# Kernel optimization log

Hardware: AMD Instinct MI355X
Metric: run time of the kernel (lower is better)

The kernel has to match this reference:

```python
import jax, jax.numpy as jnp
import numpy as np

B = 4096       # batch size
DIM = 1024     # feature dim
E = 9          # 8 session experts + 1 default layer (index 8)


def setup_inputs() -> dict:
    key = jax.random.key(0)
    k_x, k_w, k_b, k_i = jax.random.split(key, 4)
    x = jax.random.normal(k_x, (B, DIM), dtype=jnp.float32)
    # Stacked nn.Linear params: W[e] has torch layout [out, in], b[e] is [out].
    # (Original init is identity+zero bias; random values exercise the same math.)
    W = jax.random.normal(k_w, (E, DIM, DIM), dtype=jnp.float32) * (DIM ** -0.5)
    b = jax.random.normal(k_b, (E, DIM), dtype=jnp.float32)
    session_idx = jax.random.randint(k_i, (B,), 0, E, dtype=jnp.int64)
    return {"x": x, "W": W, "b": b, "session_idx": session_idx}


def reference(x, W, b, session_idx):
    # Per-sample keyed linear: out[i] = x[i] @ W[session_idx[i]].T + b[session_idx[i]].
    # Dense formulation: run every expert on every sample (E small), then select.
    # y: [B, E, DIM]
    y = jnp.einsum('bd,eod->beo', x, W) + b[None, :, :]
    out = y[jnp.arange(x.shape[0]), session_idx]  # [B, DIM]
    return out
```

## Files before the change

kernel.cpp:

```cpp
#include <hip/hip_runtime.h>
#include <hip/hip_bf16.h>

#define NE 9
#define NDIM 1024
#define BM 64
#define BN 64
#define BK 64
#define NT (NDIM / BK)
#define NSLOT_MAX 72
#define WPX 144

typedef __attribute__((ext_vector_type(8))) short bf16x8;
typedef __attribute__((ext_vector_type(4))) float f32x4;

__device__ __forceinline__ unsigned pack2_bf16(float a, float b) {
    __hip_bfloat162 h = __float22bfloat162_rn(float2{a, b});
    return *reinterpret_cast<unsigned*>(&h);
}

__device__ __forceinline__ void gload_lds16(const void* g, void* l) {
    __builtin_amdgcn_global_load_lds(
        (const __attribute__((address_space(1))) unsigned int*)g,
        (__attribute__((address_space(3))) unsigned int*)l, 16, 0, 0);
}

__global__ __launch_bounds__(256)
void prep_kernel(const float* __restrict__ W, const int* __restrict__ sidx,
                 unsigned short* __restrict__ Wb,
                 int* __restrict__ perm, int4* __restrict__ desc, int nB) {
    if (blockIdx.x == 0) {
        __shared__ int cnt[NE];
        __shared__ int cur[NE];
        int t = threadIdx.x;
        if (t < NE) cnt[t] = 0;
        __syncthreads();
        for (int i = t; i < nB; i += 256) atomicAdd(&cnt[sidx[i]], 1);
        __syncthreads();
        if (t == 0) {
            int run = 0, s = 0;
            for (int e = 0; e < NE; ++e) {
                cur[e] = run;
                int c = cnt[e];
                for (int m0 = 0; m0 < c; m0 += BM) {
                    desc[s] = make_int4(e, run + m0, min(BM, c - m0), 0);
                    ++s;
                }
                run += c;
            }
            for (; s < NSLOT_MAX; ++s) desc[s] = make_int4(-1, 0, 1, 0);
        }
        __syncthreads();
        for (int i = t; i < nB; i += 256) {
            int p = atomicAdd(&cur[sidx[i]], 1);
            perm[p] = i;
        }
    } else {
        const int NW8 = NE * NDIM * (NDIM / 8);
        const int stride = (gridDim.x - 1) * 256;
        for (int u = (blockIdx.x - 1) * 256 + threadIdx.x; u < NW8; u += stride) {
            const float4* src = (const float4*)W + 2 * (size_t)u;
            float4 a = src[0], c = src[1];
            uint4 o;
            o.x = pack2_bf16(a.x, a.y);
            o.y = pack2_bf16(a.z, a.w);
            o.z = pack2_bf16(c.x, c.y);
            o.w = pack2_bf16(c.z, c.w);
            ((uint4*)Wb)[u] = o;
        }
    }
}

__global__ __launch_bounds__(256, 4)
void gemm_kernel(const float* __restrict__ x,
                 const unsigned short* __restrict__ Wb,
                 const float* __restrict__ bias,
                 const int* __restrict__ perm,
                 const int4* __restrict__ desc,
                 float* __restrict__ out) {
    const int b    = blockIdx.x;
    const int w    = (b & 7) * WPX + (b >> 3);
    const int slot = w >> 4;
    const int n    = w & 15;
    const int4 d   = desc[slot];
    if (d.x < 0) return;
    const int e = d.x, rowstart = d.y, rcnt = d.z;
    const int n0 = n * BN;

    __shared__ __align__(16) unsigned short lds[16384];

    const int t    = threadIdx.x;
    const int wave = t >> 6;
    const int lane = t & 63;
    const int fr   = lane & 15;
    const int fq   = lane >> 4;
    const int wr   = (wave >> 1) * 32;
    const int wc   = (wave & 1) * 32;
    const int xr   = fr & 7;

    const int srow = t >> 3;
    const int c8   = t & 7;
    const int sc   = c8 ^ (srow & 7);

    int lm0 = srow;      if (lm0 >= rcnt) lm0 = rcnt - 1;
    int lm1 = srow + 32; if (lm1 >= rcnt) lm1 = rcnt - 1;
    const float* ap0 = x + (size_t)perm[rowstart + lm0] * NDIM + c8 * 8;
    const float* ap1 = x + (size_t)perm[rowstart + lm1] * NDIM + c8 * 8;
    const unsigned short* bp =
        Wb + ((size_t)e * NDIM + n0 + srow) * NDIM + sc * 8;

    float4 av[4];

#define LOADA(K0)                                                              \
    do {                                                                       \
        av[0] = *(const float4*)(ap0 + (K0));                                  \
        av[1] = *(const float4*)(ap0 + (K0) + 4);                              \
        av[2] = *(const float4*)(ap1 + (K0));                                  \
        av[3] = *(const float4*)(ap1 + (K0) + 4);                              \
    } while (0)

#define CVTA(BUF)                                                              \
    do {                                                                       \
        uint4 o0, o1;                                                          \
        o0.x = pack2_bf16(av[0].x, av[0].y);                                   \
        o0.y = pack2_bf16(av[0].z, av[0].w);                                   \
        o0.z = pack2_bf16(av[1].x, av[1].y);                                   \
        o0.w = pack2_bf16(av[1].z, av[1].w);                                   \
        o1.x = pack2_bf16(av[2].x, av[2].y);                                   \
        o1.y = pack2_bf16(av[2].z, av[2].w);                                   \
        o1.z = pack2_bf16(av[3].x, av[3].y);                                   \
        o1.w = pack2_bf16(av[3].z, av[3].w);                                   \
        *reinterpret_cast<uint4*>(&lds[(BUF) * 4096 + srow * 64 + sc * 8]) = o0;      \
        *reinterpret_cast<uint4*>(&lds[(BUF) * 4096 + (srow + 32) * 64 + sc * 8]) = o1;\
    } while (0)

#define STAGEB(BUF, K0)                                                        \
    do {                                                                       \
        gload_lds16(bp + (K0), &lds[8192 + (BUF) * 4096 + wave * 512]);        \
        gload_lds16(bp + (size_t)32 * NDIM + (K0),                             \
                    &lds[8192 + (BUF) * 4096 + 2048 + wave * 512]);            \
    } while (0)

    f32x4 acc[2][2];
#pragma unroll
    for (int i = 0; i < 2; ++i)
#pragma unroll
        for (int k = 0; k < 2; ++k) acc[i][k] = (f32x4)(0.0f);

    LOADA(0);
    STAGEB(0, 0);
    CVTA(0);
    LOADA(BK);
    __syncthreads();

    for (int tt = 0; tt < NT; ++tt) {
        const int cur = tt & 1;
        if (tt + 1 < NT) STAGEB(cur ^ 1, (tt + 1) * BK);

        const int abase = cur * 4096;
        const int bbase = 8192 + cur * 4096;
#pragma unroll
        for (int kk = 0; kk < 2; ++kk) {
            const int cs = ((kk * 4 + fq) ^ xr) * 8;
            bf16x8 af[2], bfv[2];
#pragma unroll
            for (int mf = 0; mf < 2; ++mf)
                af[mf] = *reinterpret_cast<const bf16x8*>(
                    &lds[abase + (wr + mf * 16 + fr) * 64 + cs]);
#pragma unroll
            for (int nf = 0; nf < 2; ++nf)
                bfv[nf] = *reinterpret_cast<const bf16x8*>(
                    &lds[bbase + (wc + nf * 16 + fr) * 64 + cs]);
#pragma unroll
            for (int mf = 0; mf < 2; ++mf)
#pragma unroll
                for (int nf = 0; nf < 2; ++nf)
                    acc[mf][nf] = __builtin_amdgcn_mfma_f32_16x16x32_bf16(
                        af[mf], bfv[nf], acc[mf][nf], 0, 0, 0);
        }

        if (tt + 1 < NT) {
            CVTA(cur ^ 1);
            if (tt + 2 < NT) LOADA((tt + 2) * BK);
            __syncthreads();
        }
    }
#undef LOADA
#undef CVTA
#undef STAGEB

    float bl[2];
#pragma unroll
    for (int nf = 0; nf < 2; ++nf)
        bl[nf] = bias[e * NDIM + n0 + wc + nf * 16 + fr];

#pragma unroll
    for (int mf = 0; mf < 2; ++mf) {
#pragma unroll
        for (int jr = 0; jr < 4; ++jr) {
            int lm = wr + mf * 16 + fq * 4 + jr;
            if (lm < rcnt) {
                int grow = perm[rowstart + lm];
                float* orow = out + (size_t)grow * NDIM;
#pragma unroll
                for (int nf = 0; nf < 2; ++nf)
                    orow[n0 + wc + nf * 16 + fr] = acc[mf][nf][jr] + bl[nf];
            }
        }
    }
}

__global__ void naive_kernel(const float* __restrict__ x, const float* __restrict__ W,
                             const float* __restrict__ bias,
                             const int* __restrict__ sidx, float* __restrict__ out,
                             int nB) {
    int i = blockIdx.x;
    int c = threadIdx.x + (blockIdx.y << 8);
    if (i >= nB || c >= NDIM) return;
    int e = sidx[i];
    const float* wrow = W + ((size_t)e * NDIM + c) * NDIM;
    const float* xr = x + (size_t)i * NDIM;
    float s = bias[e * NDIM + c];
    for (int k = 0; k < NDIM; ++k) s += xr[k] * wrow[k];
    out[(size_t)i * NDIM + c] = s;
}

extern "C" void kernel_launch(void* const* d_in, const int* in_sizes, int n_in,
                              void* d_out, int out_size, void* d_ws, size_t ws_size,
                              hipStream_t stream) {
    const float* x    = (const float*)d_in[0];
    const float* W    = (const float*)d_in[1];
    const float* bias = (const float*)d_in[2];
    const int*   sidx = (const int*)d_in[3];
    float*       out  = (float*)d_out;

    const int nB = in_sizes[3];

    char* wsb = (char*)d_ws;
    size_t p_desc = (size_t)nB * 4;
    size_t p_wb   = ((p_desc + NSLOT_MAX * 16 + 511) / 512) * 512;
    size_t need   = p_wb + (size_t)NE * NDIM * NDIM * 2;

    if (ws_size < need) {
        dim3 g(nB, NDIM / 256);
        naive_kernel<<<g, 256, 0, stream>>>(x, W, bias, sidx, out, nB);
        return;
    }

    int*  perm = (int*)wsb;
    int4* desc = (int4*)(wsb + p_desc);
    unsigned short* Wb = (unsigned short*)(wsb + p_wb);

    prep_kernel<<<1024, 256, 0, stream>>>(W, sidx, Wb, perm, desc, nB);

    gemm_kernel<<<NSLOT_MAX * 16, 256, 0, stream>>>(x, Wb, bias, perm, desc, out);
}
```

Baseline: 52.45 us.

## Replace LDS-staged GEMM with register-direct MFMA loads and pre-converted bf16 x

The prep kernel now also converts x to bf16 in a workspace buffer. The GEMM drops LDS staging and barriers entirely: each wave loads its MFMA operand fragments straight from global memory into registers with a two-stage software prefetch. Tiles grow to 128 rows by 64 columns, and each wave now owns 32 rows by 64 columns. This removes the LDS round trip and the syncthreads, and it halves the slot count. In exchange, operands are no longer shared across waves, so global and L2 traffic per block rises, and every load is an uncoalesced strided 16-byte fragment.

```diff
diff --git a/kernel.cpp b/kernel.cpp
--- a/kernel.cpp
+++ b/kernel.cpp
@@ -3,12 +3,9 @@
 
 #define NE 9
 #define NDIM 1024
-#define BM 64
-#define BN 64
-#define BK 64
-#define NT (NDIM / BK)
-#define NSLOT_MAX 72
-#define WPX 144
+#define SLOT_ROWS 128
+#define NSLOT_MAX 48
+#define SPX (NSLOT_MAX / 8)
 
 typedef __attribute__((ext_vector_type(8))) short bf16x8;
 typedef __attribute__((ext_vector_type(4))) float f32x4;
@@ -18,15 +15,10 @@
     return *reinterpret_cast<unsigned*>(&h);
 }
 
-__device__ __forceinline__ void gload_lds16(const void* g, void* l) {
-    __builtin_amdgcn_global_load_lds(
-        (const __attribute__((address_space(1))) unsigned int*)g,
-        (__attribute__((address_space(3))) unsigned int*)l, 16, 0, 0);
-}
-
 __global__ __launch_bounds__(256)
-void prep_kernel(const float* __restrict__ W, const int* __restrict__ sidx,
-                 unsigned short* __restrict__ Wb,
+void prep_kernel(const float* __restrict__ x, const float* __restrict__ W,
+                 const int* __restrict__ sidx,
+                 unsigned short* __restrict__ xb, unsigned short* __restrict__ Wb,
                  int* __restrict__ perm, int4* __restrict__ desc, int nB) {
     if (blockIdx.x == 0) {
         __shared__ int cnt[NE];
@@ -41,8 +33,8 @@
             for (int e = 0; e < NE; ++e) {
                 cur[e] = run;
                 int c = cnt[e];
-                for (int m0 = 0; m0 < c; m0 += BM) {
-                    desc[s] = make_int4(e, run + m0, min(BM, c - m0), 0);
+                for (int m0 = 0; m0 < c; m0 += SLOT_ROWS) {
+                    desc[s] = make_int4(e, run + m0, min(SLOT_ROWS, c - m0), 0);
                     ++s;
                 }
                 run += c;
@@ -56,154 +48,135 @@
         }
     } else {
         const int NW8 = NE * NDIM * (NDIM / 8);
+        const int NX8 = nB * (NDIM / 8);
+        const int tot = NW8 + NX8;
         const int stride = (gridDim.x - 1) * 256;
-        for (int u = (blockIdx.x - 1) * 256 + threadIdx.x; u < NW8; u += stride) {
-            const float4* src = (const float4*)W + 2 * (size_t)u;
+        for (int u = (blockIdx.x - 1) * 256 + threadIdx.x; u < tot; u += stride) {
+            const float4* src;
+            uint4* dst;
+            if (u < NW8) {
+                src = (const float4*)W + 2 * (size_t)u;
+                dst = (uint4*)Wb + u;
+            } else {
+                size_t v = (size_t)(u - NW8);
+                src = (const float4*)x + 2 * v;
+                dst = (uint4*)xb + v;
+            }
             float4 a = src[0], c = src[1];
             uint4 o;
             o.x = pack2_bf16(a.x, a.y);
             o.y = pack2_bf16(a.z, a.w);
             o.z = pack2_bf16(c.x, c.y);
             o.w = pack2_bf16(c.z, c.w);
-            ((uint4*)Wb)[u] = o;
+            *dst = o;
         }
     }
 }
 
 __global__ __launch_bounds__(256, 4)
-void gemm_kernel(const float* __restrict__ x,
-                 const unsigned short* __restrict__ Wb,
-                 const float* __restrict__ bias,
-                 const int* __restrict__ perm,
-                 const int4* __restrict__ desc,
-                 float* __restrict__ out) {
+void gemm_reg_kernel(const unsigned short* __restrict__ xb,
+                     const unsigned short* __restrict__ Wb,
+                     const float* __restrict__ bias,
+                     const int* __restrict__ perm,
+                     const int4* __restrict__ desc,
+                     float* __restrict__ out) {
     const int b    = blockIdx.x;
-    const int w    = (b & 7) * WPX + (b >> 3);
-    const int slot = w >> 4;
-    const int n    = w & 15;
+    const int xcd  = b & 7;
+    const int loc  = b >> 3;
+    const int slot = xcd * SPX + (loc >> 4);
+    const int n    = loc & 15;
     const int4 d   = desc[slot];
     if (d.x < 0) return;
     const int e = d.x, rowstart = d.y, rcnt = d.z;
-    const int n0 = n * BN;
-
-    __shared__ __align__(16) unsigned short lds[16384];
+    const int n0 = n * 64;
 
     const int t    = threadIdx.x;
     const int wave = t >> 6;
     const int lane = t & 63;
     const int fr   = lane & 15;
     const int fq   = lane >> 4;
-    const int wr   = (wave >> 1) * 32;
-    const int wc   = (wave & 1) * 32;
-    const int xr   = fr & 7;
-
-    const int srow = t >> 3;
-    const int c8   = t & 7;
-    const int sc   = c8 ^ (srow & 7);
-
-    int lm0 = srow;      if (lm0 >= rcnt) lm0 = rcnt - 1;
-    int lm1 = srow + 32; if (lm1 >= rcnt) lm1 = rcnt - 1;
-    const float* ap0 = x + (size_t)perm[rowstart + lm0] * NDIM + c8 * 8;
-    const float* ap1 = x + (size_t)perm[rowstart + lm1] * NDIM + c8 * 8;
-    const unsigned short* bp =
-        Wb + ((size_t)e * NDIM + n0 + srow) * NDIM + sc * 8;
-
-    float4 av[4];
-
-#define LOADA(K0)                                                              \
+    const int ws   = wave * 32;
+
+    const unsigned short* ap0;
+    const unsigned short* ap1;
+    {
+        int lm0 = ws + fr;      if (lm0 >= rcnt) lm0 = rcnt - 1;
+        int lm1 = ws + 16 + fr; if (lm1 >= rcnt) lm1 = rcnt - 1;
+        ap0 = xb + (size_t)perm[rowstart + lm0] * NDIM + fq * 8;
+        ap1 = xb + (size_t)perm[rowstart + lm1] * NDIM + fq * 8;
+    }
+    const unsigned short* bp0 = Wb + ((size_t)e * NDIM + n0 +      fr) * NDIM + fq * 8;
+    const unsigned short* bp1 = bp0 + (size_t)16 * NDIM;
+    const unsigned short* bp2 = bp0 + (size_t)32 * NDIM;
+    const unsigned short* bp3 = bp0 + (size_t)48 * NDIM;
+
+    f32x4 acc[2][4];
+#pragma unroll
+    for (int i = 0; i < 2; ++i)
+#pragma unroll
+        for (int k = 0; k < 4; ++k) acc[i][k] = (f32x4)(0.0f);
+
+    bf16x8 a0_0, a0_1, b0_0, b0_1, b0_2, b0_3;
+    bf16x8 a1_0, a1_1, b1_0, b1_1, b1_2, b1_3;
+
+#define LD0(KK)                                                    \
+    do {                                                           \
+        a0_0 = *(const bf16x8*)(ap0 + (KK));                       \
+        a0_1 = *(const bf16x8*)(ap1 + (KK));                       \
+        b0_0 = *(const bf16x8*)(bp0 + (KK));                       \
+        b0_1 = *(const bf16x8*)(bp1 + (KK));                       \
+        b0_2 = *(const bf16x8*)(bp2 + (KK));                       \
+        b0_3 = *(const bf16x8*)(bp3 + (KK));                       \
+    } while (0)
+#define LD1(KK)                                                    \
+    do {                                                           \
+        a1_0 = *(const bf16x8*)(ap0 + (KK));                       \
+        a1_1 = *(const bf16x8*)(ap1 + (KK));                       \
+        b1_0 = *(const bf16x8*)(bp0 + (KK));                       \
+        b1_1 = *(const bf16x8*)(bp1 + (KK));                       \
+        b1_2 = *(const bf16x8*)(bp2 + (KK));                       \
+        b1_3 = *(const bf16x8*)(bp3 + (KK));                       \
+    } while (0)
+#define MM(A0, A1, B0, B1, B2, B3)                                             \
     do {                                                                       \
-        av[0] = *(const float4*)(ap0 + (K0));                                  \
-        av[1] = *(const float4*)(ap0 + (K0) + 4);                              \
-        av[2] = *(const float4*)(ap1 + (K0));                                  \
-        av[3] = *(const float4*)(ap1 + (K0) + 4);                              \
+        acc[0][0] = __builtin_amdgcn_mfma_f32_16x16x32_bf16(A0, B0, acc[0][0], 0, 0, 0); \
+        acc[0][1] = __builtin_amdgcn_mfma_f32_16x16x32_bf16(A0, B1, acc[0][1], 0, 0, 0); \
+        acc[0][2] = __builtin_amdgcn_mfma_f32_16x16x32_bf16(A0, B2, acc[0][2], 0, 0, 0); \
+        acc[0][3] = __builtin_amdgcn_mfma_f32_16x16x32_bf16(A0, B3, acc[0][3], 0, 0, 0); \
+        acc[1][0] = __builtin_amdgcn_mfma_f32_16x16x32_bf16(A1, B0, acc[1][0], 0, 0, 0); \
+        acc[1][1] = __builtin_amdgcn_mfma_f32_16x16x32_bf16(A1, B1, acc[1][1], 0, 0, 0); \
+        acc[1][2] = __builtin_amdgcn_mfma_f32_16x16x32_bf16(A1, B2, acc[1][2], 0, 0, 0); \
+        acc[1][3] = __builtin_amdgcn_mfma_f32_16x16x32_bf16(A1, B3, acc[1][3], 0, 0, 0); \
     } while (0)
 
-#define CVTA(BUF)                                                              \
-    do {                                                                       \
-        uint4 o0, o1;                                                          \
-        o0.x = pack2_bf16(av[0].x, av[0].y);                                   \
-        o0.y = pack2_bf16(av[0].z, av[0].w);                                   \
-        o0.z = pack2_bf16(av[1].x, av[1].y);                                   \
-        o0.w = pack2_bf16(av[1].z, av[1].w);                                   \
-        o1.x = pack2_bf16(av[2].x, av[2].y);                                   \
-        o1.y = pack2_bf16(av[2].z, av[2].w);                                   \
-        o1.z = pack2_bf16(av[3].x, av[3].y);                                   \
-        o1.w = pack2_bf16(av[3].z, av[3].w);                                   \
-        *reinterpret_cast<uint4*>(&lds[(BUF) * 4096 + srow * 64 + sc * 8]) = o0;      \
-        *reinterpret_cast<uint4*>(&lds[(BUF) * 4096 + (srow + 32) * 64 + sc * 8]) = o1;\
-    } while (0)
-
-#define STAGEB(BUF, K0)                                                        \
-    do {                                                                       \
-        gload_lds16(bp + (K0), &lds[8192 + (BUF) * 4096 + wave * 512]);        \
-        gload_lds16(bp + (size_t)32 * NDIM + (K0),                             \
-                    &lds[8192 + (BUF) * 4096 + 2048 + wave * 512]);            \
-    } while (0)
-
-    f32x4 acc[2][2];
-#pragma unroll
-    for (int i = 0; i < 2; ++i)
-#pragma unroll
-        for (int k = 0; k < 2; ++k) acc[i][k] = (f32x4)(0.0f);
-
-    LOADA(0);
-    STAGEB(0, 0);
-    CVTA(0);
-    LOADA(BK);
-    __syncthreads();
-
-    for (int tt = 0; tt < NT; ++tt) {
-        const int cur = tt & 1;
-        if (tt + 1 < NT) STAGEB(cur ^ 1, (tt + 1) * BK);
-
-        const int abase = cur * 4096;
-        const int bbase = 8192 + cur * 4096;
-#pragma unroll
-        for (int kk = 0; kk < 2; ++kk) {
-            const int cs = ((kk * 4 + fq) ^ xr) * 8;
-            bf16x8 af[2], bfv[2];
-#pragma unroll
-            for (int mf = 0; mf < 2; ++mf)
-                af[mf] = *reinterpret_cast<const bf16x8*>(
-                    &lds[abase + (wr + mf * 16 + fr) * 64 + cs]);
-#pragma unroll
-            for (int nf = 0; nf < 2; ++nf)
-                bfv[nf] = *reinterpret_cast<const bf16x8*>(
-                    &lds[bbase + (wc + nf * 16 + fr) * 64 + cs]);
-#pragma unroll
-            for (int mf = 0; mf < 2; ++mf)
-#pragma unroll
-                for (int nf = 0; nf < 2; ++nf)
-                    acc[mf][nf] = __builtin_amdgcn_mfma_f32_16x16x32_bf16(
-                        af[mf], bfv[nf], acc[mf][nf], 0, 0, 0);
-        }
-
-        if (tt + 1 < NT) {
-            CVTA(cur ^ 1);
-            if (tt + 2 < NT) LOADA((tt + 2) * BK);
-            __syncthreads();
-        }
-    }
-#undef LOADA
-#undef CVTA
-#undef STAGEB
-
-    float bl[2];
-#pragma unroll
-    for (int nf = 0; nf < 2; ++nf)
-        bl[nf] = bias[e * NDIM + n0 + wc + nf * 16 + fr];
+    LD0(0);
+#pragma unroll
+    for (int kk = 0; kk < NDIM; kk += 64) {
+        LD1(kk + 32);
+        MM(a0_0, a0_1, b0_0, b0_1, b0_2, b0_3);
+        if (kk + 64 < NDIM) LD0(kk + 64);
+        MM(a1_0, a1_1, b1_0, b1_1, b1_2, b1_3);
+    }
+#undef LD0
+#undef LD1
+#undef MM
+
+    float bl[4];
+#pragma unroll
+    for (int nf = 0; nf < 4; ++nf)
+        bl[nf] = bias[e * NDIM + n0 + nf * 16 + fr];
 
 #pragma unroll
     for (int mf = 0; mf < 2; ++mf) {
 #pragma unroll
         for (int jr = 0; jr < 4; ++jr) {
-            int lm = wr + mf * 16 + fq * 4 + jr;
+            int lm = ws + mf * 16 + fq * 4 + jr;
             if (lm < rcnt) {
                 int grow = perm[rowstart + lm];
                 float* orow = out + (size_t)grow * NDIM;
 #pragma unroll
-                for (int nf = 0; nf < 2; ++nf)
-                    orow[n0 + wc + nf * 16 + fr] = acc[mf][nf][jr] + bl[nf];
+                for (int nf = 0; nf < 4; ++nf)
+                    orow[n0 + nf * 16 + fr] = acc[mf][nf][jr] + bl[nf];
             }
         }
     }
@@ -237,7 +210,8 @@
 
     char* wsb = (char*)d_ws;
     size_t p_desc = (size_t)nB * 4;
-    size_t p_wb   = ((p_desc + NSLOT_MAX * 16 + 511) / 512) * 512;
+    size_t p_xb   = ((p_desc + NSLOT_MAX * 16 + 511) / 512) * 512;
+    size_t p_wb   = p_xb + (size_t)nB * NDIM * 2;
     size_t need   = p_wb + (size_t)NE * NDIM * NDIM * 2;
 
     if (ws_size < need) {
@@ -248,9 +222,10 @@
 
     int*  perm = (int*)wsb;
     int4* desc = (int4*)(wsb + p_desc);
+    unsigned short* xb = (unsigned short*)(wsb + p_xb);
     unsigned short* Wb = (unsigned short*)(wsb + p_wb);
 
-    prep_kernel<<<1024, 256, 0, stream>>>(W, sidx, Wb, perm, desc, nB);
-
-    gemm_kernel<<<NSLOT_MAX * 16, 256, 0, stream>>>(x, Wb, bias, perm, desc, out);
-}
+    prep_kernel<<<1024, 256, 0, stream>>>(x, W, sidx, xb, Wb, perm, desc, nB);
+
+    gemm_reg_kernel<<<NSLOT_MAX * 16, 256, 0, stream>>>(xb, Wb, bias, perm, desc, out);
+}
```

Result: slower. 92.37 us (+76.1%).
